# Performance work log

Measured on AMD Instinct MI355X. Metric: run time of the kernel, lower is better.

Reference implementation:

```python
import jax, jax.numpy as jnp
import numpy as np

KERNEL_SIZE = 13
SIGMA_MIN, SIGMA_MAX = 0.4, 10.0
BETA, THRESHOLD = 0.95, 1.0


@jax.custom_vjp
def spike(x):
    # Heaviside forward, snntorch ATan surrogate backward (alpha=2)
    return (x > 0).astype(x.dtype)

def _spike_fwd(x):
    return spike(x), x

def _spike_bwd(x, g):
    return (g / (1.0 + (jnp.pi * x) ** 2),)

spike.defvjp(_spike_fwd, _spike_bwd)


def setup_inputs() -> dict:
    key = jax.random.key(0)
    k1, k2 = jax.random.split(key)
    B, C, T = 32, 224, 2048
    inp = jax.random.normal(k1, (B, 1, C, T), dtype=jnp.float32)
    linear_w = jax.random.normal(k2, (1, C), dtype=jnp.float32) * (1.0 / np.sqrt(C))
    return {"inp": inp, "linear_w": linear_w}


def _forward(inp, linear_w):
    x = inp[:, 0]  # [B, C, T]
    B, C, T = x.shape
    sigma_mean = 0.5 * (SIGMA_MIN + SIGMA_MAX)
    # adaptive sigma per (batch, time): Linear over channel axis, no bias
    w = sigma_mean + jnp.einsum('bct,c->bt', x, linear_w[0]) * (SIGMA_MAX - SIGMA_MIN)
    w = jnp.clip(w, SIGMA_MIN, SIGMA_MAX)  # [B, T]

    half = KERNEL_SIZE // 2
    r = jnp.linspace(-half, half, KERNEL_SIZE)
    r_all = jnp.linspace(-half * 10, half * 10, KERNEL_SIZE * 10)
    sig = w[..., None]  # [B, T, 1]
    kern = jnp.exp(-0.5 * (r / sig) ** 2)                       # [B, T, K]
    norm = jnp.exp(-0.5 * (r_all / sig) ** 2).sum(-1, keepdims=True)
    kern = kern / norm                                          # normalized over fine grid

    # adaptive gaussian smoothing along the CHANNEL axis (per timestep kernel)
    xt = jnp.transpose(x, (0, 2, 1))                            # [B, T, C]
    padded = jnp.pad(xt, ((0, 0), (0, 0), (half, half)))        # zero pad channels
    x_mean = sum(padded[:, :, k:k + C] * kern[:, :, k:k + 1]
                 for k in range(KERNEL_SIZE))                   # [B, T, C]
    x_mean = jnp.transpose(x_mean, (0, 2, 1))                   # [B, C, T]

    I = x - jax.nn.relu(x - x_mean)                             # soft min(x, x_mean)

    # Leaky-integrate-and-fire over time (snntorch Leaky, reset-by-subtract)
    def step(mem, I_t):
        reset = jax.lax.stop_gradient((mem > THRESHOLD).astype(I_t.dtype))
        mem = BETA * mem + I_t - reset * THRESHOLD
        spk = spike(mem - THRESHOLD)
        return mem, spk

    I_seq = jnp.transpose(I, (2, 0, 1))                         # [T, B, C]
    _, spk = jax.lax.scan(step, jnp.zeros((B, C), I.dtype), I_seq)
    spk = jnp.transpose(spk, (1, 2, 0))                         # [B, C, T]
    return spk[:, None]                                         # [B, 1, C, T]


def reference(inp, linear_w):
    return _forward(inp, linear_w)
```

## Files before the change

### kernel.cpp

```cpp
#include <hip/hip_runtime.h>
#include <math.h>

#define BB 32
#define CCH 224
#define TTT 2048
#define TPB 64
#define NT  (TTT/TPB)
#define CG  28
#define NCG (CCH/CG)
#define ROWS 40
#define XROW 68
#define IROW 29

__global__ __launch_bounds__(256) void kw(
    const float* __restrict__ x, const float* __restrict__ lw,
    double* __restrict__ kernG)
{
    const int b = blockIdx.y;
    const int t = blockIdx.x * 256 + threadIdx.x;
    const float* xb = x + (((size_t)b * CCH) << 11) + t;

    double p0 = 0, p1 = 0, p2 = 0, p3 = 0;
    #pragma unroll 8
    for (int i = 0; i < 56; ++i) {
        p0 += (double)xb[(size_t)i << 11]         * (double)lw[i];
        p1 += (double)xb[(size_t)(i + 56) << 11]  * (double)lw[i + 56];
        p2 += (double)xb[(size_t)(i + 112) << 11] * (double)lw[i + 112];
        p3 += (double)xb[(size_t)(i + 168) << 11] * (double)lw[i + 168];
    }
    double acc = (p0 + p1) + (p2 + p3);

    double w = 5.2 + acc * 9.6;
    w = fmin(fmax(w, 0.4), 10.0);
    double iw2 = 1.0 / (w * w);

    const double s = 120.0 / 129.0;
    double G  = exp(-0.125 * s * s * iw2);
    double G2 = G * G, G4 = G2 * G2, G8 = G4 * G4;
    double term = G, cmul = G8, norm = G;
    for (int u = 1; u <= 64; ++u) { term *= cmul; cmul *= G8; norm += term; }
    norm *= 2.0;

    double P = exp(-0.5 * iw2), P2 = P * P;
    double a = 1.0, bm = P, inv = 1.0 / norm;
    double* kr = kernG + (size_t)(b * TTT + t) * 7;
    kr[0] = inv;
    #pragma unroll
    for (int d = 1; d <= 6; ++d) {
        a *= bm; bm *= P2;
        kr[d] = a * inv;
    }
}

__global__ __launch_bounds__(192) void kf(
    const float* __restrict__ x, const double* __restrict__ kernG,
    float* __restrict__ out)
{
    __shared__ __align__(16) float xs[2][ROWS][XROW];
    __shared__ double kd[2][TPB][7];
    __shared__ double Is[2][TPB][IROW];
    __shared__ unsigned long long bitsb[2][CG];

    const int b   = blockIdx.y;
    const int cgi = blockIdx.x;
    const int c0  = cgi * CG;
    const int tid = threadIdx.x;
    const int ctid = tid - 64;

    const float*  xbase = x + (((size_t)(b * CCH)) << 11);
    const double* kbase = kernG + (size_t)(b * TTT) * 7;
    float* obase = out + (((size_t)(b * CCH + c0)) << 11);

    double mem = 0.0;
    bool   r   = false;

    if (tid >= 64) {
        #pragma unroll
        for (int i2 = 0; i2 < 5; ++i2) {
            int e = ctid + i2 * 128;
            int rr = e >> 4, q = e & 15;
            int cr = c0 - 6 + rr;
            float4 v = make_float4(0.f, 0.f, 0.f, 0.f);
            if (cr >= 0 && cr < CCH)
                v = *(const float4*)(xbase + ((size_t)cr << 11) + 4 * q);
            *(float4*)&xs[0][rr][4 * q] = v;
        }
        if (ctid < TPB) {
            const double* kp = kbase + (size_t)ctid * 7;
            #pragma unroll
            for (int i2 = 0; i2 < 7; ++i2) kd[0][ctid][i2] = kp[i2];
        }
    }
    __syncthreads();

    for (int k = 0; k <= NT + 1; ++k) {
        if (tid >= 64) {
            const int buf = k & 1, nbuf = (k + 1) & 1;
            float4 rv[5]; double kv[7];
            const bool st = (k + 1 <= NT - 1);
            if (st) {
                const int gt0 = (k + 1) * TPB;
                #pragma unroll
                for (int i2 = 0; i2 < 5; ++i2) {
                    int e = ctid + i2 * 128;
                    int rr = e >> 4, q = e & 15;
                    int cr = c0 - 6 + rr;
                    rv[i2] = make_float4(0.f, 0.f, 0.f, 0.f);
                    if (cr >= 0 && cr < CCH)
                        rv[i2] = *(const float4*)(xbase + ((size_t)cr << 11) + gt0 + 4 * q);
                }
                if (ctid < TPB) {
                    const double* kp = kbase + (size_t)(gt0 + ctid) * 7;
                    #pragma unroll
                    for (int i2 = 0; i2 < 7; ++i2) kv[i2] = kp[i2];
                }
            }
            if (k <= NT - 1) {
                const int t  = ctid & 63;
                const int ch = ctid >> 6;
                const int cb = 14 * ch;
                double kk7[7];
                #pragma unroll
                for (int i2 = 0; i2 < 7; ++i2) kk7[i2] = kd[buf][t][i2];
                float xv[13];
                #pragma unroll
                for (int i2 = 0; i2 < 13; ++i2) xv[i2] = xs[buf][cb + i2][t];
                #pragma unroll
                for (int c = 0; c < 14; ++c) {
                    double acc = 0.0;
                    #pragma unroll
                    for (int kk2 = 0; kk2 < 13; ++kk2) {
                        int d = kk2 < 6 ? 6 - kk2 : kk2 - 6;
                        acc = fma((double)xv[(c + kk2) % 13], kk7[d], acc);
                    }
                    double xvv = (double)xv[(c + 6) % 13];
                    double dd  = xvv - acc;
                    Is[buf][t][cb + c] = xvv - (dd > 0.0 ? dd : 0.0);
                    if (c < 13) xv[c % 13] = xs[buf][cb + c + 13][t];
                }
            }
            if (k >= 2) {
                const int j = k - 2, jb = j & 1;
                const int t0o = j * TPB;
                #pragma unroll
                for (int i2 = 0; i2 < 4; ++i2) {
                    int e = ctid + i2 * 128;
                    if (e < 448) {
                        int c = e >> 4, q = e & 15;
                        unsigned long long bits = bitsb[jb][c] >> (4 * q);
                        float4 v;
                        v.x = (bits & 1ull) ? 1.0f : 0.0f;
                        v.y = (bits & 2ull) ? 1.0f : 0.0f;
                        v.z = (bits & 4ull) ? 1.0f : 0.0f;
                        v.w = (bits & 8ull) ? 1.0f : 0.0f;
                        *(float4*)(obase + ((size_t)c << 11) + t0o + 4 * q) = v;
                    }
                }
            }
            if (st) {
                #pragma unroll
                for (int i2 = 0; i2 < 5; ++i2) {
                    int e = ctid + i2 * 128;
                    int rr = e >> 4, q = e & 15;
                    *(float4*)&xs[nbuf][rr][4 * q] = rv[i2];
                }
                if (ctid < TPB) {
                    #pragma unroll
                    for (int i2 = 0; i2 < 7; ++i2) kd[nbuf][ctid][i2] = kv[i2];
                }
            }
        } else {
            if (k >= 1 && k <= NT) {
                const int p = (k - 1) & 1;
                const int c = tid;
                if (c < CG) {
                    unsigned long long bits = 0ull;
                    double va[8], vb[8];
                    #pragma unroll
                    for (int j2 = 0; j2 < 8; ++j2) va[j2] = Is[p][j2][c];
                    #pragma unroll
                    for (int g = 0; g < 64; g += 16) {
                        #pragma unroll
                        for (int j2 = 0; j2 < 8; ++j2) vb[j2] = Is[p][g + 8 + j2][c];
                        #pragma unroll
                        for (int j2 = 0; j2 < 8; ++j2) {
                            double a2 = va[j2];
                            double cm = a2 - 1.0;
                            double m1 = fma(0.95, mem, a2);
                            double m2 = fma(0.95, mem, cm);
                            mem = r ? m2 : m1;
                            r = mem > 1.0;
                            bits |= (unsigned long long)(r ? 1 : 0) << (g + j2);
                        }
                        if (g + 16 < 64) {
                            #pragma unroll
                            for (int j2 = 0; j2 < 8; ++j2) va[j2] = Is[p][g + 16 + j2][c];
                        }
                        #pragma unroll
                        for (int j2 = 0; j2 < 8; ++j2) {
                            double a2 = vb[j2];
                            double cm = a2 - 1.0;
                            double m1 = fma(0.95, mem, a2);
                            double m2 = fma(0.95, mem, cm);
                            mem = r ? m2 : m1;
                            r = mem > 1.0;
                            bits |= (unsigned long long)(r ? 1 : 0) << (g + 8 + j2);
                        }
                    }
                    bitsb[p][c] = bits;
                }
            }
        }
        __syncthreads();
    }
}

extern "C" void kernel_launch(void* const* d_in, const int* in_sizes, int n_in,
                              void* d_out, int out_size, void* d_ws, size_t ws_size,
                              hipStream_t stream)
{
    const float* x  = (const float*)d_in[0];
    const float* lw = (const float*)d_in[1];
    float* out = (float*)d_out;

    double* kernG = (double*)d_ws;

    kw<<<dim3(TTT / 256, BB), 256, 0, stream>>>(x, lw, kernG);
    kf<<<dim3(NCG, BB), 192, 0, stream>>>(x, kernG, out);
}
```

Measured before the change: 153.1 us.

## Halve channel group size, split kw channel reduction across warps, transpose kernel weights

The main kernel now handles 14 channels per block instead of 28, which doubles the grid to 512 blocks so more of the scan work runs in parallel. Each block recomputes the same 12-row halo, so the redundant x loads rise relative to useful work. The weight kernel now splits the 224-channel dot product across four 64-thread groups and combines the partial sums through shared memory, giving four times as many blocks. Its 7-tap output is stored as seven planes of size B*T so that reads and writes are coalesced.

Result: slower. 158.7 us (+3.7%).

```diff
diff --git a/kernel.cpp b/kernel.cpp
--- a/kernel.cpp
+++ b/kernel.cpp
@@ -4,51 +4,57 @@
 #define BB 32
 #define CCH 224
 #define TTT 2048
+#define BT (BB*TTT)
 #define TPB 64
 #define NT  (TTT/TPB)
-#define CG  28
+#define CG  14
 #define NCG (CCH/CG)
-#define ROWS 40
+#define ROWS (CG+12)
 #define XROW 68
-#define IROW 29
+#define IROW 15
 
 __global__ __launch_bounds__(256) void kw(
     const float* __restrict__ x, const float* __restrict__ lw,
     double* __restrict__ kernG)
 {
-    const int b = blockIdx.y;
-    const int t = blockIdx.x * 256 + threadIdx.x;
-    const float* xb = x + (((size_t)b * CCH) << 11) + t;
-
-    double p0 = 0, p1 = 0, p2 = 0, p3 = 0;
+    __shared__ double sd[4][64];
+    const int b  = blockIdx.y;
+    const int t0 = blockIdx.x * 64;
+    const int tt = threadIdx.x & 63;
+    const int m  = threadIdx.x >> 6;
+
+    const float* xb = x + (((size_t)(b * CCH + 56 * m)) << 11) + t0 + tt;
+    double acc = 0.0;
     #pragma unroll 8
-    for (int i = 0; i < 56; ++i) {
-        p0 += (double)xb[(size_t)i << 11]         * (double)lw[i];
-        p1 += (double)xb[(size_t)(i + 56) << 11]  * (double)lw[i + 56];
-        p2 += (double)xb[(size_t)(i + 112) << 11] * (double)lw[i + 112];
-        p3 += (double)xb[(size_t)(i + 168) << 11] * (double)lw[i + 168];
-    }
-    double acc = (p0 + p1) + (p2 + p3);
-
-    double w = 5.2 + acc * 9.6;
-    w = fmin(fmax(w, 0.4), 10.0);
-    double iw2 = 1.0 / (w * w);
-
-    const double s = 120.0 / 129.0;
-    double G  = exp(-0.125 * s * s * iw2);
-    double G2 = G * G, G4 = G2 * G2, G8 = G4 * G4;
-    double term = G, cmul = G8, norm = G;
-    for (int u = 1; u <= 64; ++u) { term *= cmul; cmul *= G8; norm += term; }
-    norm *= 2.0;
-
-    double P = exp(-0.5 * iw2), P2 = P * P;
-    double a = 1.0, bm = P, inv = 1.0 / norm;
-    double* kr = kernG + (size_t)(b * TTT + t) * 7;
-    kr[0] = inv;
-    #pragma unroll
-    for (int d = 1; d <= 6; ++d) {
-        a *= bm; bm *= P2;
-        kr[d] = a * inv;
+    for (int i = 0; i < 56; ++i)
+        acc += (double)xb[(size_t)i << 11] * (double)lw[56 * m + i];
+    sd[m][tt] = acc;
+    __syncthreads();
+
+    if (threadIdx.x < 64) {
+        const int t = threadIdx.x;
+        double s2 = (sd[0][t] + sd[1][t]) + (sd[2][t] + sd[3][t]);
+
+        double w = 5.2 + s2 * 9.6;
+        w = fmin(fmax(w, 0.4), 10.0);
+        double iw2 = 1.0 / (w * w);
+
+        const double s = 120.0 / 129.0;
+        double G  = exp(-0.125 * s * s * iw2);
+        double G2 = G * G, G4 = G2 * G2, G8 = G4 * G4;
+        double term = G, cmul = G8, norm = G;
+        for (int u = 1; u <= 64; ++u) { term *= cmul; cmul *= G8; norm += term; }
+        norm *= 2.0;
+
+        double P = exp(-0.5 * iw2), P2 = P * P;
+        double a = 1.0, bm = P, inv = 1.0 / norm;
+        double* kr = kernG + (size_t)b * TTT + t0 + t;
+        kr[0] = inv;
+        #pragma unroll
+        for (int d = 1; d <= 6; ++d) {
+            a *= bm; bm *= P2;
+            kr[(size_t)d * BT] = a * inv;
+        }
     }
 }
 
@@ -68,7 +74,7 @@
     const int ctid = tid - 64;
 
     const float*  xbase = x + (((size_t)(b * CCH)) << 11);
-    const double* kbase = kernG + (size_t)(b * TTT) * 7;
+    const double* kbase = kernG + (size_t)b * TTT;
     float* obase = out + (((size_t)(b * CCH + c0)) << 11);
 
     double mem = 0.0;
@@ -76,19 +82,21 @@
 
     if (tid >= 64) {
         #pragma unroll
-        for (int i2 = 0; i2 < 5; ++i2) {
+        for (int i2 = 0; i2 < 4; ++i2) {
             int e = ctid + i2 * 128;
-            int rr = e >> 4, q = e & 15;
-            int cr = c0 - 6 + rr;
-            float4 v = make_float4(0.f, 0.f, 0.f, 0.f);
-            if (cr >= 0 && cr < CCH)
-                v = *(const float4*)(xbase + ((size_t)cr << 11) + 4 * q);
-            *(float4*)&xs[0][rr][4 * q] = v;
+            if (e < ROWS * 16) {
+                int rr = e >> 4, q = e & 15;
+                int cr = c0 - 6 + rr;
+                float4 v = make_float4(0.f, 0.f, 0.f, 0.f);
+                if (cr >= 0 && cr < CCH)
+                    v = *(const float4*)(xbase + ((size_t)cr << 11) + 4 * q);
+                *(float4*)&xs[0][rr][4 * q] = v;
+            }
         }
         if (ctid < TPB) {
-            const double* kp = kbase + (size_t)ctid * 7;
             #pragma unroll
-            for (int i2 = 0; i2 < 7; ++i2) kd[0][ctid][i2] = kp[i2];
+            for (int d = 0; d < 7; ++d)
+                kd[0][ctid][d] = kbase[(size_t)d * BT + ctid];
         }
     }
     __syncthreads();
@@ -96,29 +104,31 @@
     for (int k = 0; k <= NT + 1; ++k) {
         if (tid >= 64) {
             const int buf = k & 1, nbuf = (k + 1) & 1;
-            float4 rv[5]; double kv[7];
+            float4 rv[4]; double kv[7];
             const bool st = (k + 1 <= NT - 1);
             if (st) {
                 const int gt0 = (k + 1) * TPB;
                 #pragma unroll
-                for (int i2 = 0; i2 < 5; ++i2) {
+                for (int i2 = 0; i2 < 4; ++i2) {
                     int e = ctid + i2 * 128;
-                    int rr = e >> 4, q = e & 15;
-                    int cr = c0 - 6 + rr;
                     rv[i2] = make_float4(0.f, 0.f, 0.f, 0.f);
-                    if (cr >= 0 && cr < CCH)
-                        rv[i2] = *(const float4*)(xbase + ((size_t)cr << 11) + gt0 + 4 * q);
+                    if (e < ROWS * 16) {
+                        int rr = e >> 4, q = e & 15;
+                        int cr = c0 - 6 + rr;
+                        if (cr >= 0 && cr < CCH)
+                            rv[i2] = *(const float4*)(xbase + ((size_t)cr << 11) + gt0 + 4 * q);
+                    }
                 }
                 if (ctid < TPB) {
-                    const double* kp = kbase + (size_t)(gt0 + ctid) * 7;
-                    #pragma unroll
-                    for (int i2 = 0; i2 < 7; ++i2) kv[i2] = kp[i2];
+                    #pragma unroll
+                    for (int d = 0; d < 7; ++d)
+                        kv[d] = kbase[(size_t)d * BT + gt0 + ctid];
                 }
             }
             if (k <= NT - 1) {
                 const int t  = ctid & 63;
                 const int ch = ctid >> 6;
-                const int cb = 14 * ch;
+                const int cb = 7 * ch;
                 double kk7[7];
                 #pragma unroll
                 for (int i2 = 0; i2 < 7; ++i2) kk7[i2] = kd[buf][t][i2];
@@ -126,7 +136,7 @@
                 #pragma unroll
                 for (int i2 = 0; i2 < 13; ++i2) xv[i2] = xs[buf][cb + i2][t];
                 #pragma unroll
-                for (int c = 0; c < 14; ++c) {
+                for (int c = 0; c < 7; ++c) {
                     double acc = 0.0;
                     #pragma unroll
                     for (int kk2 = 0; kk2 < 13; ++kk2) {
@@ -136,16 +146,16 @@
                     double xvv = (double)xv[(c + 6) % 13];
                     double dd  = xvv - acc;
                     Is[buf][t][cb + c] = xvv - (dd > 0.0 ? dd : 0.0);
-                    if (c < 13) xv[c % 13] = xs[buf][cb + c + 13][t];
+                    if (c < 6) xv[c % 13] = xs[buf][cb + c + 13][t];
                 }
             }
             if (k >= 2) {
                 const int j = k - 2, jb = j & 1;
                 const int t0o = j * TPB;
                 #pragma unroll
-                for (int i2 = 0; i2 < 4; ++i2) {
+                for (int i2 = 0; i2 < 2; ++i2) {
                     int e = ctid + i2 * 128;
-                    if (e < 448) {
+                    if (e < CG * 16) {
                         int c = e >> 4, q = e & 15;
                         unsigned long long bits = bitsb[jb][c] >> (4 * q);
                         float4 v;
@@ -159,14 +169,16 @@
             }
             if (st) {
                 #pragma unroll
-                for (int i2 = 0; i2 < 5; ++i2) {
+                for (int i2 = 0; i2 < 4; ++i2) {
                     int e = ctid + i2 * 128;
-                    int rr = e >> 4, q = e & 15;
-                    *(float4*)&xs[nbuf][rr][4 * q] = rv[i2];
+                    if (e < ROWS * 16) {
+                        int rr = e >> 4, q = e & 15;
+                        *(float4*)&xs[nbuf][rr][4 * q] = rv[i2];
+                    }
                 }
                 if (ctid < TPB) {
                     #pragma unroll
-                    for (int i2 = 0; i2 < 7; ++i2) kd[nbuf][ctid][i2] = kv[i2];
+                    for (int d = 0; d < 7; ++d) kd[nbuf][ctid][d] = kv[d];
                 }
             }
         } else {
@@ -225,6 +237,6 @@
 
     double* kernG = (double*)d_ws;
 
-    kw<<<dim3(TTT / 256, BB), 256, 0, stream>>>(x, lw, kernG);
+    kw<<<dim3(TTT / 64, BB), 256, 0, stream>>>(x, lw, kernG);
     kf<<<dim3(NCG, BB), 192, 0, stream>>>(x, kernG, out);
 }
```

## Replace block barriers with flag-based producer/consumer sync and register-prefetched inputs

Applied to the files above, without the earlier changes.

The smoothing kernel drops the per-tile __syncthreads barrier and shared-memory staging of x and kernel weights. Compute waves now prefetch their 26 channel rows and 7 weights directly into registers, and coordinate with the LIF-scan wave through workgroup-scope acquire/release flags in shared memory with sleep-spin waits. The goal is to let the serial scan wave and the convolution waves run decoupled instead of lockstepping on barriers. The kernel-weight workspace is changed to a structure-of-arrays layout, and the weight kernel now uses float4 loads split across four waves with a shared-memory reduction. This adds register pressure and spin-wait overhead, and the flag protocol could deadlock or race if the indices are off.

After: 174.3 us. 13.9% more time.

```diff
diff --git a/kernel.cpp b/kernel.cpp
--- a/kernel.cpp
+++ b/kernel.cpp
@@ -4,51 +4,72 @@
 #define BB 32
 #define CCH 224
 #define TTT 2048
+#define BT (BB*TTT)
 #define TPB 64
 #define NT  (TTT/TPB)
 #define CG  28
 #define NCG (CCH/CG)
-#define ROWS 40
-#define XROW 68
 #define IROW 29
+
+#define PF(s,h) ((s)*2+(h))
+#define CF(s)   (4+(s))
+#define SF(s)   (6+(s))
+#define OF(s,h) (8+(s)*2+(h))
 
 __global__ __launch_bounds__(256) void kw(
     const float* __restrict__ x, const float* __restrict__ lw,
     double* __restrict__ kernG)
 {
-    const int b = blockIdx.y;
-    const int t = blockIdx.x * 256 + threadIdx.x;
-    const float* xb = x + (((size_t)b * CCH) << 11) + t;
-
-    double p0 = 0, p1 = 0, p2 = 0, p3 = 0;
-    #pragma unroll 8
-    for (int i = 0; i < 56; ++i) {
-        p0 += (double)xb[(size_t)i << 11]         * (double)lw[i];
-        p1 += (double)xb[(size_t)(i + 56) << 11]  * (double)lw[i + 56];
-        p2 += (double)xb[(size_t)(i + 112) << 11] * (double)lw[i + 112];
-        p3 += (double)xb[(size_t)(i + 168) << 11] * (double)lw[i + 168];
+    __shared__ double sd[4][256];
+    __shared__ float  lws[CCH];
+    const int b   = blockIdx.y;
+    const int t0  = blockIdx.x * 256;
+    const int tid = threadIdx.x;
+
+    if (tid < CCH) lws[tid] = lw[tid];
+    __syncthreads();
+
+    {
+        const int q = tid & 63, m = tid >> 6;
+        const float* xb = x + (((size_t)(b * CCH + 56 * m)) << 11) + t0 + 4 * q;
+        double a0 = 0, a1 = 0, a2 = 0, a3 = 0;
+        #pragma unroll 8
+        for (int i = 0; i < 56; ++i) {
+            float4 v = *(const float4*)(xb + ((size_t)i << 11));
+            double wv = (double)lws[56 * m + i];
+            a0 += (double)v.x * wv;
+            a1 += (double)v.y * wv;
+            a2 += (double)v.z * wv;
+            a3 += (double)v.w * wv;
+        }
+        sd[m][4 * q + 0] = a0; sd[m][4 * q + 1] = a1;
+        sd[m][4 * q + 2] = a2; sd[m][4 * q + 3] = a3;
     }
-    double acc = (p0 + p1) + (p2 + p3);
-
-    double w = 5.2 + acc * 9.6;
-    w = fmin(fmax(w, 0.4), 10.0);
-    double iw2 = 1.0 / (w * w);
-
-    const double s = 120.0 / 129.0;
-    double G  = exp(-0.125 * s * s * iw2);
-    double G2 = G * G, G4 = G2 * G2, G8 = G4 * G4;
-    double term = G, cmul = G8, norm = G;
-    for (int u = 1; u <= 64; ++u) { term *= cmul; cmul *= G8; norm += term; }
-    norm *= 2.0;
-
-    double P = exp(-0.5 * iw2), P2 = P * P;
-    double a = 1.0, bm = P, inv = 1.0 / norm;
-    double* kr = kernG + (size_t)(b * TTT + t) * 7;
-    kr[0] = inv;
-    #pragma unroll
-    for (int d = 1; d <= 6; ++d) {
-        a *= bm; bm *= P2;
-        kr[d] = a * inv;
+    __syncthreads();
+
+    {
+        double s2 = (sd[0][tid] + sd[1][tid]) + (sd[2][tid] + sd[3][tid]);
+
+        double w = 5.2 + s2 * 9.6;
+        w = fmin(fmax(w, 0.4), 10.0);
+        double iw2 = 1.0 / (w * w);
+
+        const double s = 120.0 / 129.0;
+        double G  = exp(-0.125 * s * s * iw2);
+        double G2 = G * G, G4 = G2 * G2, G8 = G4 * G4;
+        double term = G, cmul = G8, norm = G;
+        for (int u = 1; u <= 64; ++u) { term *= cmul; cmul *= G8; norm += term; }
+        norm *= 2.0;
+
+        double P = exp(-0.5 * iw2), P2 = P * P;
+        double a = 1.0, bm = P, inv = 1.0 / norm;
+        double* kr = kernG + (size_t)b * TTT + t0 + tid;
+        kr[0] = inv;
+        #pragma unroll
+        for (int d = 1; d <= 6; ++d) {
+            a *= bm; bm *= P2;
+            kr[(size_t)d * BT] = a * inv;
+        }
     }
 }
 
@@ -56,162 +77,174 @@
     const float* __restrict__ x, const double* __restrict__ kernG,
     float* __restrict__ out)
 {
-    __shared__ __align__(16) float xs[2][ROWS][XROW];
-    __shared__ double kd[2][TPB][7];
     __shared__ double Is[2][TPB][IROW];
     __shared__ unsigned long long bitsb[2][CG];
-
-    const int b   = blockIdx.y;
-    const int cgi = blockIdx.x;
-    const int c0  = cgi * CG;
-    const int tid = threadIdx.x;
-    const int ctid = tid - 64;
+    __shared__ int fl[16];
+
+    const int b    = blockIdx.y;
+    const int c0   = blockIdx.x * CG;
+    const int tid  = threadIdx.x;
+    const int wid  = tid >> 6;
+    const int lane = tid & 63;
+
+    if (tid < 16) fl[tid] = 0;
+    __syncthreads();
 
     const float*  xbase = x + (((size_t)(b * CCH)) << 11);
-    const double* kbase = kernG + (size_t)(b * TTT) * 7;
+    const double* kbase = kernG + (size_t)b * TTT;
     float* obase = out + (((size_t)(b * CCH + c0)) << 11);
 
-    double mem = 0.0;
-    bool   r   = false;
-
-    if (tid >= 64) {
+    if (wid >= 1) {
+        const int h  = wid - 1;
+        const int cb = 14 * h;
+        const int crow0 = c0 + cb - 6;
+        float  xc[26], xn[26];
+        double kc[7],  kn[7];
+
         #pragma unroll
-        for (int i2 = 0; i2 < 5; ++i2) {
-            int e = ctid + i2 * 128;
-            int rr = e >> 4, q = e & 15;
-            int cr = c0 - 6 + rr;
-            float4 v = make_float4(0.f, 0.f, 0.f, 0.f);
-            if (cr >= 0 && cr < CCH)
-                v = *(const float4*)(xbase + ((size_t)cr << 11) + 4 * q);
-            *(float4*)&xs[0][rr][4 * q] = v;
-        }
-        if (ctid < TPB) {
-            const double* kp = kbase + (size_t)ctid * 7;
-            #pragma unroll
-            for (int i2 = 0; i2 < 7; ++i2) kd[0][ctid][i2] = kp[i2];
-        }
-    }
-    __syncthreads();
-
-    for (int k = 0; k <= NT + 1; ++k) {
-        if (tid >= 64) {
-            const int buf = k & 1, nbuf = (k + 1) & 1;
-            float4 rv[5]; double kv[7];
-            const bool st = (k + 1 <= NT - 1);
-            if (st) {
-                const int gt0 = (k + 1) * TPB;
-                #pragma unroll
-                for (int i2 = 0; i2 < 5; ++i2) {
-                    int e = ctid + i2 * 128;
-                    int rr = e >> 4, q = e & 15;
-                    int cr = c0 - 6 + rr;
-                    rv[i2] = make_float4(0.f, 0.f, 0.f, 0.f);
-                    if (cr >= 0 && cr < CCH)
-                        rv[i2] = *(const float4*)(xbase + ((size_t)cr << 11) + gt0 + 4 * q);
-                }
-                if (ctid < TPB) {
-                    const double* kp = kbase + (size_t)(gt0 + ctid) * 7;
-                    #pragma unroll
-                    for (int i2 = 0; i2 < 7; ++i2) kv[i2] = kp[i2];
-                }
+        for (int i = 0; i < 26; ++i) {
+            int cr = crow0 + i;
+            xc[i] = (cr >= 0 && cr < CCH) ? xbase[((size_t)cr << 11) + lane] : 0.0f;
+        }
+        #pragma unroll
+        for (int d = 0; d < 7; ++d) kc[d] = kbase[(size_t)d * BT + lane];
+
+        #pragma unroll 1
+        for (int k = 0; k <= NT + 1; ++k) {
+            if (k + 1 <= NT - 1) {
+                const int gt = (k + 1) * TPB + lane;
+                #pragma unroll
+                for (int i = 0; i < 26; ++i) {
+                    int cr = crow0 + i;
+                    xn[i] = (cr >= 0 && cr < CCH) ? xbase[((size_t)cr << 11) + gt] : 0.0f;
+                }
+                #pragma unroll
+                for (int d = 0; d < 7; ++d) kn[d] = kbase[(size_t)d * BT + gt];
             }
             if (k <= NT - 1) {
-                const int t  = ctid & 63;
-                const int ch = ctid >> 6;
-                const int cb = 14 * ch;
-                double kk7[7];
-                #pragma unroll
-                for (int i2 = 0; i2 < 7; ++i2) kk7[i2] = kd[buf][t][i2];
-                float xv[13];
-                #pragma unroll
-                for (int i2 = 0; i2 < 13; ++i2) xv[i2] = xs[buf][cb + i2][t];
+                const int s = k & 1;
+                while (__hip_atomic_load(&fl[CF(s)], __ATOMIC_ACQUIRE,
+                                         __HIP_MEMORY_SCOPE_WORKGROUP) < k - 1)
+                    __builtin_amdgcn_s_sleep(1);
                 #pragma unroll
                 for (int c = 0; c < 14; ++c) {
                     double acc = 0.0;
                     #pragma unroll
-                    for (int kk2 = 0; kk2 < 13; ++kk2) {
-                        int d = kk2 < 6 ? 6 - kk2 : kk2 - 6;
-                        acc = fma((double)xv[(c + kk2) % 13], kk7[d], acc);
-                    }
-                    double xvv = (double)xv[(c + 6) % 13];
+                    for (int kk = 0; kk < 13; ++kk) {
+                        int d = kk < 6 ? 6 - kk : kk - 6;
+                        acc = fma((double)xc[c + kk], kc[d], acc);
+                    }
+                    double xvv = (double)xc[c + 6];
                     double dd  = xvv - acc;
-                    Is[buf][t][cb + c] = xvv - (dd > 0.0 ? dd : 0.0);
-                    if (c < 13) xv[c % 13] = xs[buf][cb + c + 13][t];
-                }
-            }
-            if (k >= 2) {
-                const int j = k - 2, jb = j & 1;
-                const int t0o = j * TPB;
-                #pragma unroll
-                for (int i2 = 0; i2 < 4; ++i2) {
-                    int e = ctid + i2 * 128;
-                    if (e < 448) {
-                        int c = e >> 4, q = e & 15;
-                        unsigned long long bits = bitsb[jb][c] >> (4 * q);
+                    Is[s][lane][cb + c] = xvv - (dd > 0.0 ? dd : 0.0);
+                }
+                if (lane == 0)
+                    __hip_atomic_store(&fl[PF(s, h)], k + 1, __ATOMIC_RELEASE,
+                                       __HIP_MEMORY_SCOPE_WORKGROUP);
+            }
+            const int j = k - 2;
+            if (j >= 0) {
+                const int s2 = j & 1;
+                while (__hip_atomic_load(&fl[SF(s2)], __ATOMIC_ACQUIRE,
+                                         __HIP_MEMORY_SCOPE_WORKGROUP) < j + 1)
+                    __builtin_amdgcn_s_sleep(1);
+                unsigned long long bb[4];
+                #pragma unroll
+                for (int i = 0; i < 4; ++i) {
+                    int e = lane + (i << 6);
+                    int cl = (e < 224) ? (e >> 4) : 13;
+                    bb[i] = bitsb[s2][cb + cl];
+                }
+                if (lane == 0)
+                    __hip_atomic_store(&fl[OF(s2, h)], j + 1, __ATOMIC_RELEASE,
+                                       __HIP_MEMORY_SCOPE_WORKGROUP);
+                #pragma unroll
+                for (int i = 0; i < 4; ++i) {
+                    int e = lane + (i << 6);
+                    if (e < 224) {
+                        int cl = e >> 4, qq = e & 15;
+                        unsigned long long bv = bb[i] >> (4 * qq);
                         float4 v;
-                        v.x = (bits & 1ull) ? 1.0f : 0.0f;
-                        v.y = (bits & 2ull) ? 1.0f : 0.0f;
-                        v.z = (bits & 4ull) ? 1.0f : 0.0f;
-                        v.w = (bits & 8ull) ? 1.0f : 0.0f;
-                        *(float4*)(obase + ((size_t)c << 11) + t0o + 4 * q) = v;
-                    }
-                }
-            }
-            if (st) {
-                #pragma unroll
-                for (int i2 = 0; i2 < 5; ++i2) {
-                    int e = ctid + i2 * 128;
-                    int rr = e >> 4, q = e & 15;
-                    *(float4*)&xs[nbuf][rr][4 * q] = rv[i2];
-                }
-                if (ctid < TPB) {
-                    #pragma unroll
-                    for (int i2 = 0; i2 < 7; ++i2) kd[nbuf][ctid][i2] = kv[i2];
-                }
-            }
-        } else {
-            if (k >= 1 && k <= NT) {
-                const int p = (k - 1) & 1;
-                const int c = tid;
-                if (c < CG) {
-                    unsigned long long bits = 0ull;
-                    double va[8], vb[8];
-                    #pragma unroll
-                    for (int j2 = 0; j2 < 8; ++j2) va[j2] = Is[p][j2][c];
-                    #pragma unroll
-                    for (int g = 0; g < 64; g += 16) {
+                        v.x = (bv & 1ull) ? 1.0f : 0.0f;
+                        v.y = (bv & 2ull) ? 1.0f : 0.0f;
+                        v.z = (bv & 4ull) ? 1.0f : 0.0f;
+                        v.w = (bv & 8ull) ? 1.0f : 0.0f;
+                        *(float4*)(obase + ((size_t)(cb + cl) << 11) + j * TPB + 4 * qq) = v;
+                    }
+                }
+            }
+            if (k + 1 <= NT - 1) {
+                #pragma unroll
+                for (int i = 0; i < 26; ++i) xc[i] = xn[i];
+                #pragma unroll
+                for (int d = 0; d < 7; ++d) kc[d] = kn[d];
+            }
+        }
+    } else {
+        const int c    = lane;
+        const int cidx = (c < CG) ? c : 0;
+        double mem = 0.0;
+        bool   r   = false;
+
+        #pragma unroll 1
+        for (int k = 0; k < NT; ++k) {
+            const int s = k & 1;
+            while (__hip_atomic_load(&fl[PF(s, 0)], __ATOMIC_ACQUIRE,
+                                     __HIP_MEMORY_SCOPE_WORKGROUP) < k + 1 ||
+                   __hip_atomic_load(&fl[PF(s, 1)], __ATOMIC_ACQUIRE,
+                                     __HIP_MEMORY_SCOPE_WORKGROUP) < k + 1)
+                __builtin_amdgcn_s_sleep(1);
+
+            unsigned long long bits = 0ull;
+            {
+                double va[8], vb[8];
+                #pragma unroll
+                for (int j2 = 0; j2 < 8; ++j2) va[j2] = Is[s][j2][cidx];
+                #pragma unroll
+                for (int g = 0; g < 64; g += 16) {
+                    #pragma unroll
+                    for (int j2 = 0; j2 < 8; ++j2) vb[j2] = Is[s][g + 8 + j2][cidx];
+                    #pragma unroll
+                    for (int j2 = 0; j2 < 8; ++j2) {
+                        double a2 = va[j2];
+                        double cm = a2 - 1.0;
+                        double m1 = fma(0.95, mem, a2);
+                        double m2 = fma(0.95, mem, cm);
+                        mem = r ? m2 : m1;
+                        r = mem > 1.0;
+                        bits |= (unsigned long long)(r ? 1 : 0) << (g + j2);
+                    }
+                    if (g + 16 < 64) {
                         #pragma unroll
-                        for (int j2 = 0; j2 < 8; ++j2) vb[j2] = Is[p][g + 8 + j2][c];
-                        #pragma unroll
-                        for (int j2 = 0; j2 < 8; ++j2) {
-                            double a2 = va[j2];
-                            double cm = a2 - 1.0;
-                            double m1 = fma(0.95, mem, a2);
-                            double m2 = fma(0.95, mem, cm);
-                            mem = r ? m2 : m1;
-                            r = mem > 1.0;
-                            bits |= (unsigned long long)(r ? 1 : 0) << (g + j2);
-                        }
-                        if (g + 16 < 64) {
-                            #pragma unroll
-                            for (int j2 = 0; j2 < 8; ++j2) va[j2] = Is[p][g + 16 + j2][c];
-                        }
-                        #pragma unroll
-                        for (int j2 = 0; j2 < 8; ++j2) {
-                            double a2 = vb[j2];
-                            double cm = a2 - 1.0;
-                            double m1 = fma(0.95, mem, a2);
-                            double m2 = fma(0.95, mem, cm);
-                            mem = r ? m2 : m1;
-                            r = mem > 1.0;
-                            bits |= (unsigned long long)(r ? 1 : 0) << (g + 8 + j2);
-                        }
-                    }
-                    bitsb[p][c] = bits;
-                }
-            }
-        }
-        __syncthreads();
+                        for (int j2 = 0; j2 < 8; ++j2) va[j2] = Is[s][g + 16 + j2][cidx];
+                    }
+                    #pragma unroll
+                    for (int j2 = 0; j2 < 8; ++j2) {
+                        double a2 = vb[j2];
+                        double cm = a2 - 1.0;
+                        double m1 = fma(0.95, mem, a2);
+                        double m2 = fma(0.95, mem, cm);
+                        mem = r ? m2 : m1;
+                        r = mem > 1.0;
+                        bits |= (unsigned long long)(r ? 1 : 0) << (g + 8 + j2);
+                    }
+                }
+            }
+            if (lane == 0)
+                __hip_atomic_store(&fl[CF(s)], k + 1, __ATOMIC_RELEASE,
+                                   __HIP_MEMORY_SCOPE_WORKGROUP);
+
+            const int s2 = k & 1;
+            while (__hip_atomic_load(&fl[OF(s2, 0)], __ATOMIC_ACQUIRE,
+                                     __HIP_MEMORY_SCOPE_WORKGROUP) < k - 1 ||
+                   __hip_atomic_load(&fl[OF(s2, 1)], __ATOMIC_ACQUIRE,
+                                     __HIP_MEMORY_SCOPE_WORKGROUP) < k - 1)
+                __builtin_amdgcn_s_sleep(1);
+            if (c < CG) bitsb[s2][c] = bits;
+            if (lane == 0)
+                __hip_atomic_store(&fl[SF(s2)], k + 1, __ATOMIC_RELEASE,
+                                   __HIP_MEMORY_SCOPE_WORKGROUP);
+        }
     }
 }
 
```
